# Optimization experiments

Measured on AMD Instinct MI355X. Metric: run time of the kernel, lower is better.

## Reference

```python
import jax, jax.numpy as jnp
import numpy as np

MARGIN = 0.5        # contrastive margin (init kwarg)
NUM_LABELS = 20     # label ids are in [0, NUM_LABELS)


def setup_inputs() -> dict:
    key = jax.random.key(0)
    k1, k2 = jax.random.split(key)
    emb = jax.random.normal(k1, (4, 16, 64, 64), dtype=jnp.float32)
    lab = jax.random.randint(k2, (4, 64, 64), 0, NUM_LABELS, dtype=jnp.int32)
    return {"emb": emb, "lab": lab}


def _loss_one(x, y):
    # x: (C, H, W) embedding, y: (H, W) int labels
    C, H, W = x.shape
    N = H * W
    xf = x.reshape(C, N)
    # per-pixel centering across channels, then L2-normalize across channels
    xc = xf - jnp.mean(xf, axis=0, keepdims=True)
    nrm = jnp.sqrt(jnp.sum(xc * xc, axis=0))           # (N,)
    denom = jnp.where(nrm > 0, nrm, 1.0)
    e = jnp.where(nrm > 0, xc / denom, 0.0).T          # (N, C); NaN-mask -> 0
    sim = (e @ e.T) * 0.5 + 0.5                        # (N, N) in [0, 1]

    yi = y.reshape(N)
    yf = yi.astype(jnp.float32) + 1.0
    eq = yf[:, None] == yf[None, :]
    nz = (yf[:, None] * yf[None, :]) != 0.0            # product-zero exclusion (faithful)
    lp = jnp.where(nz, jnp.where(eq, 1.0, -1.0), 0.0)  # label-pair matrix

    # inverse-frequency per-pixel weights, outer product for pairs
    cnt = jnp.zeros((NUM_LABELS,), jnp.float32).at[yi].add(1.0)
    wpix = 1.0 / cnt[yi]                               # (N,)
    Wm = wpix[:, None] * wpix[None, :]                 # (N, N)

    # positive pairs: relu(1 - sim); negative pairs: relu(sim - margin)
    loss = jnp.where(lp == 1.0, jnp.maximum(1.0 - sim, 0.0),
                     jnp.where(lp == -1.0, jnp.maximum(sim - MARGIN, 0.0), 0.0))
    return jnp.sum(Wm * loss) / N


def reference(emb, lab):
    return jnp.sum(jax.vmap(_loss_one)(emb, lab))
```

## Files before the change

kernel.cpp:

```cpp
#include <hip/hip_runtime.h>

#define NUM_LABELS 20
#define N_PIX 4096
#define C_DIM 16
#define BATCH 4

#define PTILE 128
#define PNT (N_PIX / PTILE)
#define PTPAIRS (PNT * (PNT + 1) / 2)
#define NPAIRBLK (BATCH * PTPAIRS)

#define PREP_SLICES 16
#define NPREP (BATCH * PREP_SLICES)
#define KPAD 24

typedef __attribute__((ext_vector_type(8))) short bf16x8;
typedef __attribute__((ext_vector_type(4))) float f32x4;

__device__ __forceinline__ unsigned int bf16rne(float f) {
    unsigned int x = __float_as_uint(f);
    return (x + 0x7fffu + ((x >> 16) & 1u)) >> 16;
}

__global__ __launch_bounds__(256) void prep_kernel(
    const float* __restrict__ emb,
    const int*   __restrict__ lab,
    unsigned short* __restrict__ gT,
    float* __restrict__ sliceSq,
    float* __restrict__ presF)
{
    const int blk = blockIdx.x;
    const int b  = blk / PREP_SLICES;
    const int sl = blk % PREP_SLICES;
    const int t  = threadIdx.x;
    const int wv = t >> 6;
    const int lane = t & 63;

    __shared__ int   hist[4][NUM_LABELS];
    __shared__ float rinv[NUM_LABELS];
    __shared__ float xt[C_DIM][256];
    __shared__ float wsum[4];

    for (int i = t; i < 4 * NUM_LABELS; i += 256) (&hist[0][0])[i] = 0;
    __syncthreads();

    const int* yb = lab + (size_t)b * N_PIX;
    for (int n = t; n < N_PIX; n += 256) atomicAdd(&hist[wv][yb[n]], 1);

    const float* xb = emb + (size_t)b * C_DIM * N_PIX + sl * 256;
#pragma unroll
    for (int c = 0; c < C_DIM; ++c) xt[c][t] = xb[(size_t)c * N_PIX + t];
    __syncthreads();

    if (t < NUM_LABELS) {
        const int c = hist[0][t] + hist[1][t] + hist[2][t] + hist[3][t];
        rinv[t] = (c > 0) ? 1.0f / (float)c : 0.0f;
    }
    __syncthreads();

    if (sl == 0 && t == 0) {
        int p = 0;
#pragma unroll
        for (int l = 0; l < NUM_LABELS; ++l)
            p += (rinv[l] > 0.f) ? 1 : 0;
        presF[b] = (float)p;
    }

    const int n = sl * 256 + t;
    float v[C_DIM];
    float s = 0.f;
#pragma unroll
    for (int c = 0; c < C_DIM; ++c) { v[c] = xt[c][t]; s += v[c]; }
    const float mean = s * (1.0f / C_DIM);
    float ss = 0.f;
#pragma unroll
    for (int c = 0; c < C_DIM; ++c) { v[c] -= mean; ss += v[c] * v[c]; }
    const float nrm = sqrtf(ss);
    const float w   = rinv[yb[n]];
    const float inv = (nrm > 0.f) ? (w / nrm) : 0.f;

    unsigned int u[8];
#pragma unroll
    for (int k = 0; k < 8; ++k) {
        const unsigned int lo = bf16rne(v[2 * k] * inv);
        const unsigned int hi = bf16rne(v[2 * k + 1] * inv);
        u[k] = lo | (hi << 16);
    }
    unsigned int* gp = (unsigned int*)(gT + ((size_t)b * N_PIX + n) * C_DIM);
    *reinterpret_cast<uint4*>(gp)     = make_uint4(u[0], u[1], u[2], u[3]);
    *reinterpret_cast<uint4*>(gp + 4) = make_uint4(u[4], u[5], u[6], u[7]);

    float sq = inv * inv * ss;
#pragma unroll
    for (int off = 32; off > 0; off >>= 1) sq += __shfl_down(sq, off);
    if (lane == 0) wsum[wv] = sq;
    __syncthreads();
    if (t == 0) sliceSq[blk] = wsum[0] + wsum[1] + wsum[2] + wsum[3];
}

__global__ __launch_bounds__(256) void pair_kernel(
    const unsigned short* __restrict__ gT,
    const int*   __restrict__ lab,
    float* __restrict__ partials)
{
    const int k0 = blockIdx.x % PTPAIRS;
    const int b  = blockIdx.x / PTPAIRS;

    const float nn = (float)PNT;
    int ti = (int)(((2.f * nn + 1.f) -
                    sqrtf((2.f * nn + 1.f) * (2.f * nn + 1.f) - 8.f * (float)k0)) * 0.5f);
    if (ti < 0) ti = 0;
    if (ti > PNT - 1) ti = PNT - 1;
    auto rowoff = [](int r) { return r * PNT - (r * (r - 1)) / 2; };
    while (ti > 0 && k0 < rowoff(ti)) --ti;
    while (ti < PNT - 1 && k0 >= rowoff(ti + 1)) ++ti;
    const int tj = ti + (k0 - rowoff(ti));
    const bool diag = (ti == tj);

    __shared__ unsigned short sI[PTILE * KPAD];
    __shared__ unsigned short sJ[PTILE * KPAD];
    __shared__ int syI[PTILE], syJ[PTILE];

    const int t = threadIdx.x;
    const unsigned short* gb = gT + (size_t)b * N_PIX * C_DIM;

    {
        const int row = t >> 1, half = t & 1;
        const uint4 vI = *(reinterpret_cast<const uint4*>(gb + (size_t)(ti * PTILE + row) * C_DIM) + half);
        const uint4 vJ = *(reinterpret_cast<const uint4*>(gb + (size_t)(tj * PTILE + row) * C_DIM) + half);
        *reinterpret_cast<uint4*>(&sI[row * KPAD + half * 8]) = vI;
        *reinterpret_cast<uint4*>(&sJ[row * KPAD + half * 8]) = vJ;
    }
    if (t < PTILE) {
        syI[t] = lab[(size_t)b * N_PIX + ti * PTILE + t];
    } else {
        const int u = t - PTILE;
        syJ[u] = lab[(size_t)b * N_PIX + tj * PTILE + u];
    }
    __syncthreads();

    const int wv   = t >> 6;
    const int lane = t & 63;
    const int lo16 = lane & 15;
    const int hi   = lane >> 4;
    const bool doread = (hi < 2);

    bf16x8 afrag[2] = {bf16x8{}, bf16x8{}};
    int    yIr[2][4];
#pragma unroll
    for (int rt = 0; rt < 2; ++rt) {
        const int rtile = wv * 2 + rt;
        if (doread)
            afrag[rt] = *reinterpret_cast<const bf16x8*>(&sI[(rtile * 16 + lo16) * KPAD + hi * 8]);
        const int4 yv = *reinterpret_cast<const int4*>(&syI[rtile * 16 + hi * 4]);
        yIr[rt][0] = yv.x; yIr[rt][1] = yv.y; yIr[rt][2] = yv.z; yIr[rt][3] = yv.w;
    }

    float sum = 0.f;
#pragma unroll
    for (int ct = 0; ct < 8; ++ct) {
        bf16x8 bfrag = bf16x8{};
        if (doread)
            bfrag = *reinterpret_cast<const bf16x8*>(&sJ[(ct * 16 + lo16) * KPAD + hi * 8]);
        const int yq = syJ[ct * 16 + lo16];
#pragma unroll
        for (int rt = 0; rt < 2; ++rt) {
            const int rtile = wv * 2 + rt;
            if (diag && rtile > ct) continue;
            f32x4 acc = {0.f, 0.f, 0.f, 0.f};
            acc = __builtin_amdgcn_mfma_f32_16x16x32_bf16(afrag[rt], bfrag, acc, 0, 0, 0);
            if (diag && rtile == ct) {
#pragma unroll
                for (int j = 0; j < 4; ++j) {
                    const float s = acc[j];
                    const float r = fmaxf(s, 0.f);
                    const float v = (yIr[rt][j] == yq) ? -s : r;
                    const int iloc = hi * 4 + j;
                    sum += (iloc < lo16) ? v : 0.f;
                }
            } else {
#pragma unroll
                for (int j = 0; j < 4; ++j) {
                    const float s = acc[j];
                    const float r = fmaxf(s, 0.f);
                    sum += (yIr[rt][j] == yq) ? -s : r;
                }
            }
        }
    }

#pragma unroll
    for (int off = 32; off > 0; off >>= 1) sum += __shfl_down(sum, off);
    __shared__ float wred[4];
    if (lane == 0) wred[wv] = sum;
    __syncthreads();
    if (t == 0) partials[blockIdx.x] = wred[0] + wred[1] + wred[2] + wred[3];
}

__global__ __launch_bounds__(256) void reduce_kernel(
    const float* __restrict__ partials,
    const float* __restrict__ sliceSq,
    const float* __restrict__ presF,
    float* __restrict__ out)
{
    __shared__ double sd[256];
    const int t = threadIdx.x;
    double s = 0.0;
    for (int i = t; i < NPAIRBLK; i += 256) s += (double)partials[i];
    if (t < NPREP) s -= 0.5 * (double)sliceSq[t];
    if (t < BATCH) s += 0.5 * (double)presF[t];
    sd[t] = s;
    __syncthreads();
#pragma unroll
    for (int k = 128; k > 0; k >>= 1) {
        if (t < k) sd[t] += sd[t + k];
        __syncthreads();
    }
    if (t == 0) out[0] = (float)(sd[0] * (1.0 / (double)N_PIX));
}

extern "C" void kernel_launch(void* const* d_in, const int* in_sizes, int n_in,
                              void* d_out, int out_size, void* d_ws, size_t ws_size,
                              hipStream_t stream) {
    const float* emb = (const float*)d_in[0];
    const int*   lab = (const int*)d_in[1];
    float* out = (float*)d_out;

    unsigned short* gT = (unsigned short*)d_ws;
    float* sliceSq  = (float*)(gT + (size_t)BATCH * N_PIX * C_DIM);
    float* presF    = sliceSq + NPREP;
    float* partials = presF + BATCH;

    prep_kernel<<<NPREP, 256, 0, stream>>>(emb, lab, gT, sliceSq, presF);
    pair_kernel<<<NPAIRBLK, 256, 0, stream>>>(gT, lab, partials);
    reduce_kernel<<<1, 256, 0, stream>>>(partials, sliceSq, presF, out);
}
```

Measured before the change: 22.58 us.

## Fuse prep, pair and reduce into one cooperative kernel with grid sync

Merges the three kernels into a single cooperative launch of 704 persistent blocks. Each block processes three tile pairs and recomputes the centered, normalized bf16 embeddings for its tiles straight from the input. Every block also rebuilds the label histograms for all batches in shared memory. A grid-wide sync then lets block 0 sum the partials. This removes two kernel launches and the gT round-trip through global memory, at the cost of redundant histogram and normalization work and the overhead of a grid barrier.

Result: slower. 85.78 us (+279.9%).

```diff
diff --git a/kernel.cpp b/kernel.cpp
--- a/kernel.cpp
+++ b/kernel.cpp
@@ -1,4 +1,7 @@
 #include <hip/hip_runtime.h>
+#include <hip/hip_cooperative_groups.h>
+
+namespace cg = cooperative_groups;
 
 #define NUM_LABELS 20
 #define N_PIX 4096
@@ -8,10 +11,9 @@
 #define PTILE 128
 #define PNT (N_PIX / PTILE)
 #define PTPAIRS (PNT * (PNT + 1) / 2)
-#define NPAIRBLK (BATCH * PTPAIRS)
-
-#define PREP_SLICES 16
-#define NPREP (BATCH * PREP_SLICES)
+#define NPAIRS (BATCH * PTPAIRS)
+#define NBLK 704
+#define PAIRS_PER_BLK 3
 #define KPAD 24
 
 typedef __attribute__((ext_vector_type(8))) short bf16x8;
@@ -22,168 +24,141 @@
     return (x + 0x7fffu + ((x >> 16) & 1u)) >> 16;
 }
 
-__global__ __launch_bounds__(256) void prep_kernel(
+__global__ __launch_bounds__(256, 3) void fused_kernel(
     const float* __restrict__ emb,
     const int*   __restrict__ lab,
-    unsigned short* __restrict__ gT,
-    float* __restrict__ sliceSq,
-    float* __restrict__ presF)
+    float* __restrict__ partials,
+    float* __restrict__ out)
 {
-    const int blk = blockIdx.x;
-    const int b  = blk / PREP_SLICES;
-    const int sl = blk % PREP_SLICES;
-    const int t  = threadIdx.x;
-    const int wv = t >> 6;
+    const int bk   = blockIdx.x;
+    const int t    = threadIdx.x;
     const int lane = t & 63;
-
-    __shared__ int   hist[4][NUM_LABELS];
-    __shared__ float rinv[NUM_LABELS];
-    __shared__ float xt[C_DIM][256];
-    __shared__ float wsum[4];
-
-    for (int i = t; i < 4 * NUM_LABELS; i += 256) (&hist[0][0])[i] = 0;
-    __syncthreads();
-
-    const int* yb = lab + (size_t)b * N_PIX;
-    for (int n = t; n < N_PIX; n += 256) atomicAdd(&hist[wv][yb[n]], 1);
-
-    const float* xb = emb + (size_t)b * C_DIM * N_PIX + sl * 256;
-#pragma unroll
-    for (int c = 0; c < C_DIM; ++c) xt[c][t] = xb[(size_t)c * N_PIX + t];
-    __syncthreads();
-
-    if (t < NUM_LABELS) {
-        const int c = hist[0][t] + hist[1][t] + hist[2][t] + hist[3][t];
-        rinv[t] = (c > 0) ? 1.0f / (float)c : 0.0f;
-    }
-    __syncthreads();
-
-    if (sl == 0 && t == 0) {
-        int p = 0;
-#pragma unroll
-        for (int l = 0; l < NUM_LABELS; ++l)
-            p += (rinv[l] > 0.f) ? 1 : 0;
-        presF[b] = (float)p;
-    }
-
-    const int n = sl * 256 + t;
-    float v[C_DIM];
-    float s = 0.f;
-#pragma unroll
-    for (int c = 0; c < C_DIM; ++c) { v[c] = xt[c][t]; s += v[c]; }
-    const float mean = s * (1.0f / C_DIM);
-    float ss = 0.f;
-#pragma unroll
-    for (int c = 0; c < C_DIM; ++c) { v[c] -= mean; ss += v[c] * v[c]; }
-    const float nrm = sqrtf(ss);
-    const float w   = rinv[yb[n]];
-    const float inv = (nrm > 0.f) ? (w / nrm) : 0.f;
-
-    unsigned int u[8];
-#pragma unroll
-    for (int k = 0; k < 8; ++k) {
-        const unsigned int lo = bf16rne(v[2 * k] * inv);
-        const unsigned int hi = bf16rne(v[2 * k + 1] * inv);
-        u[k] = lo | (hi << 16);
-    }
-    unsigned int* gp = (unsigned int*)(gT + ((size_t)b * N_PIX + n) * C_DIM);
-    *reinterpret_cast<uint4*>(gp)     = make_uint4(u[0], u[1], u[2], u[3]);
-    *reinterpret_cast<uint4*>(gp + 4) = make_uint4(u[4], u[5], u[6], u[7]);
-
-    float sq = inv * inv * ss;
-#pragma unroll
-    for (int off = 32; off > 0; off >>= 1) sq += __shfl_down(sq, off);
-    if (lane == 0) wsum[wv] = sq;
-    __syncthreads();
-    if (t == 0) sliceSq[blk] = wsum[0] + wsum[1] + wsum[2] + wsum[3];
-}
-
-__global__ __launch_bounds__(256) void pair_kernel(
-    const unsigned short* __restrict__ gT,
-    const int*   __restrict__ lab,
-    float* __restrict__ partials)
-{
-    const int k0 = blockIdx.x % PTPAIRS;
-    const int b  = blockIdx.x / PTPAIRS;
-
-    const float nn = (float)PNT;
-    int ti = (int)(((2.f * nn + 1.f) -
-                    sqrtf((2.f * nn + 1.f) * (2.f * nn + 1.f) - 8.f * (float)k0)) * 0.5f);
-    if (ti < 0) ti = 0;
-    if (ti > PNT - 1) ti = PNT - 1;
-    auto rowoff = [](int r) { return r * PNT - (r * (r - 1)) / 2; };
-    while (ti > 0 && k0 < rowoff(ti)) --ti;
-    while (ti < PNT - 1 && k0 >= rowoff(ti + 1)) ++ti;
-    const int tj = ti + (k0 - rowoff(ti));
-    const bool diag = (ti == tj);
-
+    const int wv   = t >> 6;
+
+    __shared__ int   hist[BATCH][NUM_LABELS];
+    __shared__ float rinv[BATCH][NUM_LABELS];
     __shared__ unsigned short sI[PTILE * KPAD];
     __shared__ unsigned short sJ[PTILE * KPAD];
-    __shared__ int syI[PTILE], syJ[PTILE];
-
-    const int t = threadIdx.x;
-    const unsigned short* gb = gT + (size_t)b * N_PIX * C_DIM;
-
-    {
-        const int row = t >> 1, half = t & 1;
-        const uint4 vI = *(reinterpret_cast<const uint4*>(gb + (size_t)(ti * PTILE + row) * C_DIM) + half);
-        const uint4 vJ = *(reinterpret_cast<const uint4*>(gb + (size_t)(tj * PTILE + row) * C_DIM) + half);
-        *reinterpret_cast<uint4*>(&sI[row * KPAD + half * 8]) = vI;
-        *reinterpret_cast<uint4*>(&sJ[row * KPAD + half * 8]) = vJ;
-    }
-    if (t < PTILE) {
-        syI[t] = lab[(size_t)b * N_PIX + ti * PTILE + t];
-    } else {
-        const int u = t - PTILE;
-        syJ[u] = lab[(size_t)b * N_PIX + tj * PTILE + u];
-    }
-    __syncthreads();
-
-    const int wv   = t >> 6;
-    const int lane = t & 63;
-    const int lo16 = lane & 15;
-    const int hi   = lane >> 4;
-    const bool doread = (hi < 2);
-
-    bf16x8 afrag[2] = {bf16x8{}, bf16x8{}};
-    int    yIr[2][4];
-#pragma unroll
-    for (int rt = 0; rt < 2; ++rt) {
-        const int rtile = wv * 2 + rt;
-        if (doread)
-            afrag[rt] = *reinterpret_cast<const bf16x8*>(&sI[(rtile * 16 + lo16) * KPAD + hi * 8]);
-        const int4 yv = *reinterpret_cast<const int4*>(&syI[rtile * 16 + hi * 4]);
-        yIr[rt][0] = yv.x; yIr[rt][1] = yv.y; yIr[rt][2] = yv.z; yIr[rt][3] = yv.w;
-    }
+    __shared__ int   syI[PTILE], syJ[PTILE];
+    __shared__ float wred[4];
+    __shared__ double sd[256];
+
+    for (int i = t; i < BATCH * NUM_LABELS; i += 256) (&hist[0][0])[i] = 0;
+    __syncthreads();
+#pragma unroll
+    for (int b = 0; b < BATCH; ++b)
+        for (int n = t; n < N_PIX; n += 256)
+            atomicAdd(&hist[b][lab[b * N_PIX + n]], 1);
+    __syncthreads();
+    if (t < BATCH * NUM_LABELS) {
+        const int c = (&hist[0][0])[t];
+        (&rinv[0][0])[t] = (c > 0) ? 1.0f / (float)c : 0.0f;
+    }
+    __syncthreads();
 
     float sum = 0.f;
-#pragma unroll
-    for (int ct = 0; ct < 8; ++ct) {
-        bf16x8 bfrag = bf16x8{};
-        if (doread)
-            bfrag = *reinterpret_cast<const bf16x8*>(&sJ[(ct * 16 + lo16) * KPAD + hi * 8]);
-        const int yq = syJ[ct * 16 + lo16];
+    if (bk == 0 && t == 0) {
+        int p = 0;
+#pragma unroll
+        for (int i = 0; i < BATCH * NUM_LABELS; ++i) p += ((&hist[0][0])[i] > 0) ? 1 : 0;
+        sum += 0.5f * (float)p;
+    }
+
+    for (int pi = 0; pi < PAIRS_PER_BLK; ++pi) {
+        const int p  = bk + pi * NBLK;
+        const int b  = p / PTPAIRS;
+        const int k0 = p % PTPAIRS;
+
+        const float nn = (float)PNT;
+        int ti = (int)(((2.f * nn + 1.f) -
+                        sqrtf((2.f * nn + 1.f) * (2.f * nn + 1.f) - 8.f * (float)k0)) * 0.5f);
+        if (ti < 0) ti = 0;
+        if (ti > PNT - 1) ti = PNT - 1;
+        auto rowoff = [](int r) { return r * PNT - (r * (r - 1)) / 2; };
+        while (ti > 0 && k0 < rowoff(ti)) --ti;
+        while (ti < PNT - 1 && k0 >= rowoff(ti + 1)) ++ti;
+        const int tj = ti + (k0 - rowoff(ti));
+        const bool diag = (ti == tj);
+
+        __syncthreads();
+
+        {
+            const int side = t >> 7;
+            const int row  = t & 127;
+            const int tile = side ? tj : ti;
+            const int gidx = b * N_PIX + tile * PTILE + row;
+            const float* xb = emb + (size_t)b * C_DIM * N_PIX + tile * PTILE + row;
+
+            float v[C_DIM];
+            float s = 0.f;
+#pragma unroll
+            for (int c = 0; c < C_DIM; ++c) { v[c] = xb[(size_t)c * N_PIX]; s += v[c]; }
+            const float mean = s * (1.0f / C_DIM);
+            float ss = 0.f;
+#pragma unroll
+            for (int c = 0; c < C_DIM; ++c) { v[c] -= mean; ss += v[c] * v[c]; }
+            const float nrm = sqrtf(ss);
+            const int   y   = lab[gidx];
+            const float w   = rinv[b][y];
+            const float inv = (nrm > 0.f) ? (w / nrm) : 0.f;
+
+            unsigned int u[8];
+#pragma unroll
+            for (int k = 0; k < 8; ++k) {
+                const unsigned int lo = bf16rne(v[2 * k] * inv);
+                const unsigned int hi = bf16rne(v[2 * k + 1] * inv);
+                u[k] = lo | (hi << 16);
+            }
+            unsigned short* dst = side ? sJ : sI;
+            *reinterpret_cast<uint4*>(&dst[row * KPAD])     = make_uint4(u[0], u[1], u[2], u[3]);
+            *reinterpret_cast<uint4*>(&dst[row * KPAD + 8]) = make_uint4(u[4], u[5], u[6], u[7]);
+            (side ? syJ : syI)[row] = y;
+
+            if (diag && side == 0) sum -= 0.5f * (inv * inv * ss);
+        }
+        __syncthreads();
+
+        const int lo16 = lane & 15;
+        const int hi   = lane >> 4;
+        const bool doread = (hi < 2);
+
+        bf16x8 afrag[2] = {bf16x8{}, bf16x8{}};
+        int    yIr[2][4];
 #pragma unroll
         for (int rt = 0; rt < 2; ++rt) {
             const int rtile = wv * 2 + rt;
-            if (diag && rtile > ct) continue;
-            f32x4 acc = {0.f, 0.f, 0.f, 0.f};
-            acc = __builtin_amdgcn_mfma_f32_16x16x32_bf16(afrag[rt], bfrag, acc, 0, 0, 0);
-            if (diag && rtile == ct) {
-#pragma unroll
-                for (int j = 0; j < 4; ++j) {
-                    const float s = acc[j];
-                    const float r = fmaxf(s, 0.f);
-                    const float v = (yIr[rt][j] == yq) ? -s : r;
-                    const int iloc = hi * 4 + j;
-                    sum += (iloc < lo16) ? v : 0.f;
-                }
-            } else {
-#pragma unroll
-                for (int j = 0; j < 4; ++j) {
-                    const float s = acc[j];
-                    const float r = fmaxf(s, 0.f);
-                    sum += (yIr[rt][j] == yq) ? -s : r;
+            if (doread)
+                afrag[rt] = *reinterpret_cast<const bf16x8*>(&sI[(rtile * 16 + lo16) * KPAD + hi * 8]);
+            const int4 yv = *reinterpret_cast<const int4*>(&syI[rtile * 16 + hi * 4]);
+            yIr[rt][0] = yv.x; yIr[rt][1] = yv.y; yIr[rt][2] = yv.z; yIr[rt][3] = yv.w;
+        }
+
+#pragma unroll
+        for (int ct = 0; ct < 8; ++ct) {
+            bf16x8 bfrag = bf16x8{};
+            if (doread)
+                bfrag = *reinterpret_cast<const bf16x8*>(&sJ[(ct * 16 + lo16) * KPAD + hi * 8]);
+            const int yq = syJ[ct * 16 + lo16];
+#pragma unroll
+            for (int rt = 0; rt < 2; ++rt) {
+                const int rtile = wv * 2 + rt;
+                if (diag && rtile > ct) continue;
+                f32x4 acc = {0.f, 0.f, 0.f, 0.f};
+                acc = __builtin_amdgcn_mfma_f32_16x16x32_bf16(afrag[rt], bfrag, acc, 0, 0, 0);
+                if (diag && rtile == ct) {
+#pragma unroll
+                    for (int j = 0; j < 4; ++j) {
+                        const float s = acc[j];
+                        const float v = (yIr[rt][j] == yq) ? -s : fmaxf(s, 0.f);
+                        const int iloc = hi * 4 + j;
+                        sum += (iloc < lo16) ? v : 0.f;
+                    }
+                } else {
+#pragma unroll
+                    for (int j = 0; j < 4; ++j) {
+                        const float s = acc[j];
+                        sum += (yIr[rt][j] == yq) ? -s : fmaxf(s, 0.f);
+                    }
                 }
             }
         }
@@ -191,32 +166,24 @@
 
 #pragma unroll
     for (int off = 32; off > 0; off >>= 1) sum += __shfl_down(sum, off);
-    __shared__ float wred[4];
     if (lane == 0) wred[wv] = sum;
     __syncthreads();
-    if (t == 0) partials[blockIdx.x] = wred[0] + wred[1] + wred[2] + wred[3];
-}
-
-__global__ __launch_bounds__(256) void reduce_kernel(
-    const float* __restrict__ partials,
-    const float* __restrict__ sliceSq,
-    const float* __restrict__ presF,
-    float* __restrict__ out)
-{
-    __shared__ double sd[256];
-    const int t = threadIdx.x;
-    double s = 0.0;
-    for (int i = t; i < NPAIRBLK; i += 256) s += (double)partials[i];
-    if (t < NPREP) s -= 0.5 * (double)sliceSq[t];
-    if (t < BATCH) s += 0.5 * (double)presF[t];
-    sd[t] = s;
-    __syncthreads();
-#pragma unroll
-    for (int k = 128; k > 0; k >>= 1) {
-        if (t < k) sd[t] += sd[t + k];
+    if (t == 0) partials[bk] = wred[0] + wred[1] + wred[2] + wred[3];
+
+    cg::this_grid().sync();
+
+    if (bk == 0) {
+        double s = 0.0;
+        for (int i = t; i < NBLK; i += 256) s += (double)partials[i];
+        sd[t] = s;
         __syncthreads();
-    }
-    if (t == 0) out[0] = (float)(sd[0] * (1.0 / (double)N_PIX));
+#pragma unroll
+        for (int k = 128; k > 0; k >>= 1) {
+            if (t < k) sd[t] += sd[t + k];
+            __syncthreads();
+        }
+        if (t == 0) out[0] = (float)(sd[0] * (1.0 / (double)N_PIX));
+    }
 }
 
 extern "C" void kernel_launch(void* const* d_in, const int* in_sizes, int n_in,
@@ -225,13 +192,9 @@
     const float* emb = (const float*)d_in[0];
     const int*   lab = (const int*)d_in[1];
     float* out = (float*)d_out;
-
-    unsigned short* gT = (unsigned short*)d_ws;
-    float* sliceSq  = (float*)(gT + (size_t)BATCH * N_PIX * C_DIM);
-    float* presF    = sliceSq + NPREP;
-    float* partials = presF + BATCH;
-
-    prep_kernel<<<NPREP, 256, 0, stream>>>(emb, lab, gT, sliceSq, presF);
-    pair_kernel<<<NPAIRBLK, 256, 0, stream>>>(gT, lab, partials);
-    reduce_kernel<<<1, 256, 0, stream>>>(partials, sliceSq, presF, out);
+    float* partials = (float*)d_ws;
+
+    void* args[] = {(void*)&emb, (void*)&lab, (void*)&partials, (void*)&out};
+    hipLaunchCooperativeKernel((const void*)fused_kernel,
+                               dim3(NBLK), dim3(256), args, 0, stream);
 }
```
